# Kernel optimization log

Measured on AMD Instinct MI355X. Metric: run time of the kernel, lower is better.

The kernel has to match this reference:

```python
import jax, jax.numpy as jnp
import numpy as np

B, T, N = 8, 100, 100000
MARGIN = 0.1
THRESHOLD = 0.5
BIG = 1.0e9


def setup_inputs() -> dict:
    key = jax.random.key(0)
    k0, k1, k2, k3, k4 = jax.random.split(key, 5)
    outputs = jax.random.normal(k0, (B, T, 3), dtype=jnp.float32)
    c2ws = jax.random.normal(k1, (B, 4, 4), dtype=jnp.float32)
    scene_scales = jax.random.uniform(k2, (B,), dtype=jnp.float32)
    means = jax.random.normal(k3, (N, 3), dtype=jnp.float32)
    scales = jax.random.uniform(k4, (N, 3), dtype=jnp.float32)
    return {"outputs": outputs, "c2ws": c2ws, "scene_scales": scene_scales,
            "means": means, "scales": scales}


def reference(outputs, c2ws, scene_scales, means, scales):
    # per-splat max radius (precomputed in torch __init__)
    maxsplatrad = jnp.max(scales, axis=1)                      # [N]
    # world transform: aff = R * scene_scale, trans = translation
    aff = c2ws[:, :3, :3] * scene_scales[:, None, None]        # [B,3,3]
    trans = c2ws[:, :3, 3]                                     # [B,3]
    # baddbmm(trans, outputs, aff.mT) == outputs @ aff^T + trans
    retrajs = jnp.einsum('btd,bed->bte', outputs, aff) + trans[:, None, :]  # [B,T,3]
    # axis-aligned bbox of each trajectory, expanded by threshold
    thres = THRESHOLD * scene_scales[0]
    uvals = jnp.max(retrajs, axis=1) + thres                   # [B,3]
    lvals = jnp.min(retrajs, axis=1) - thres                   # [B,3]
    # bbox filter: which splats fall inside each trajectory bbox
    inside = jnp.all((means[None, :, :] >= lvals[:, None, :]) &
                     (means[None, :, :] <= uvals[:, None, :]), axis=2)  # [B,N]
    # pairwise distances via ||a-b||^2 = |a|^2 + |b|^2 - 2 a.b (avoids [B,T,N,3])
    r2 = jnp.sum(retrajs * retrajs, axis=-1)                   # [B,T]
    m2 = jnp.sum(means * means, axis=-1)                       # [N]
    cross = jnp.einsum('btd,nd->btn', retrajs, means)          # [B,T,N]
    d2 = r2[:, :, None] + m2[None, None, :] - 2.0 * cross
    dist = jnp.sqrt(jnp.maximum(d2, 0.0))
    resdists = dist - maxsplatrad[None, None, :] - MARGIN      # [B,T,N]
    # scatter_reduce amin with include_self=False and 1e9 default ==
    # masked min over splats; pairs not inside bbox never scattered -> BIG
    masked = jnp.where(inside[:, None, :], resdists, BIG)
    collosses = jnp.min(masked, axis=2)                        # [B,T]
    return jnp.sum(jax.nn.relu(-collosses)) / (B * T)
```

## Files before the change

kernel.cpp:

```cpp
#include <hip/hip_runtime.h>

constexpr int   B_ = 8;
constexpr int   T_ = 100;
constexpr int   NPAIRS = B_ * T_;
constexpr int   N_ = 100000;
constexpr float MARGIN_ = 0.1f;
constexpr float THRESHOLD_ = 0.5f;
constexpr float BIG_ = 1000000000.0f;

constexpr int PER   = 98;
constexpr int NBLK  = 1024;
constexpr int NSLOT = 1024;
constexpr int KCH   = 16;
constexpr int NRED  = NBLK / KCH;

constexpr size_t RES_OFF  = 0;
constexpr size_t KEYS_OFF = RES_OFF + (size_t)NBLK * NSLOT * 4;
constexpr size_t CNT_OFF  = KEYS_OFF + (size_t)NSLOT * 4;

__device__ __forceinline__ float fsqrt(float x) { return __builtin_amdgcn_sqrtf(x); }

__device__ __forceinline__ unsigned fkey(float f) {
    unsigned u = __float_as_uint(f);
    return (u & 0x80000000u) ? ~u : (u | 0x80000000u);
}

__global__ __launch_bounds__(256) void k_main(const float* __restrict__ outputs,
                                              const float* __restrict__ c2ws,
                                              const float* __restrict__ ss,
                                              const float* __restrict__ means,
                                              const float* __restrict__ scales,
                                              char* __restrict__ ws) {
    __shared__ float  re_s[NPAIRS * 3];
    __shared__ float  bounds_s[48];
    __shared__ float4 rec_s[PER * 3];
    int tid = threadIdx.x;

    if (blockIdx.x == 0) {
        unsigned* keys = (unsigned*)(ws + KEYS_OFF);
        keys[tid]       = fkey(BIG_);
        keys[tid + 256] = fkey(BIG_);
        keys[tid + 512] = fkey(BIG_);
        keys[tid + 768] = fkey(BIG_);
        if (tid == 0) *(unsigned*)(ws + CNT_OFF) = 0;
    }

    for (int p = tid; p < NPAIRS; p += 256) {
        int b = p / T_;
        float s = ss[b];
        const float* o = outputs + p * 3;
        float o0 = o[0], o1 = o[1], o2 = o[2];
        const float* c = c2ws + b * 16;
#pragma unroll
        for (int e = 0; e < 3; e++) {
            re_s[p * 3 + e] =
                (o0 * c[e * 4 + 0] + o1 * c[e * 4 + 1] + o2 * c[e * 4 + 2]) * s + c[e * 4 + 3];
        }
    }
    __syncthreads();

    if (tid < 24) {
        int b = tid / 3, e = tid - b * 3;
        float mx = -3.4e38f, mn = 3.4e38f;
        for (int t = 0; t < T_; t++) {
            float v = re_s[(b * T_ + t) * 3 + e];
            mx = fmaxf(mx, v);
            mn = fminf(mn, v);
        }
        float thres = THRESHOLD_ * ss[0];
        bounds_s[b * 3 + e]      = mn - thres;
        bounds_s[24 + b * 3 + e] = mx + thres;
    }
    __syncthreads();

    float4 q0, q1, q2, q3;
    {
        float4* qs[4] = {&q0, &q1, &q2, &q3};
#pragma unroll
        for (int j = 0; j < 4; j++) {
            int g = tid + j * 256;
            int bb = g >> 7, r = g & 127;
            float4 q = make_float4(0.f, 0.f, 0.f, 0.f);
            if (r < T_) {
                int p = bb * T_ + r;
                q = make_float4(re_s[p * 3 + 0], re_s[p * 3 + 1], re_s[p * 3 + 2], 0.f);
            }
            *qs[j] = q;
        }
    }
    if (tid < PER) {
        int n = blockIdx.x * PER + tid;
        float mx = 0.f, my = 0.f, mz = 0.f;
        float e0, e1, e2, e3, e4, e5, e6, e7;
        if (n < N_) {
            mx = means[(size_t)n * 3 + 0];
            my = means[(size_t)n * 3 + 1];
            mz = means[(size_t)n * 3 + 2];
            float msr = fmaxf(fmaxf(scales[(size_t)n * 3 + 0], scales[(size_t)n * 3 + 1]),
                              scales[(size_t)n * 3 + 2]) + MARGIN_;
            float e[8];
#pragma unroll
            for (int b = 0; b < 8; b++) {
                bool in = (mx >= bounds_s[b * 3 + 0]) & (mx <= bounds_s[24 + b * 3 + 0]) &
                          (my >= bounds_s[b * 3 + 1]) & (my <= bounds_s[24 + b * 3 + 1]) &
                          (mz >= bounds_s[b * 3 + 2]) & (mz <= bounds_s[24 + b * 3 + 2]);
                e[b] = in ? msr : -BIG_;
            }
            e0 = e[0]; e1 = e[1]; e2 = e[2]; e3 = e[3];
            e4 = e[4]; e5 = e[5]; e6 = e[6]; e7 = e[7];
        } else {
            e0 = e1 = e2 = e3 = e4 = e5 = e6 = e7 = -BIG_;
        }
        rec_s[tid * 3 + 0] = make_float4(mx, my, mz, 0.f);
        rec_s[tid * 3 + 1] = make_float4(e0, e2, e4, e6);
        rec_s[tid * 3 + 2] = make_float4(e1, e3, e5, e7);
    }
    __syncthreads();

    int effidx = 1 + ((__builtin_amdgcn_readfirstlane(tid) >> 7) & 1);

    float mn0 = BIG_, mn1 = BIG_, mn2 = BIG_, mn3 = BIG_;
#pragma unroll 2
    for (int i = 0; i < PER; i++) {
        float4 pos = rec_s[i * 3];
        float4 ef  = rec_s[i * 3 + effidx];
        float dx, dy, dz, d2;
        dx = q0.x - pos.x; dy = q0.y - pos.y; dz = q0.z - pos.z;
        d2 = fmaf(dz, dz, fmaf(dy, dy, dx * dx));
        mn0 = fminf(mn0, fsqrt(d2) - ef.x);
        dx = q1.x - pos.x; dy = q1.y - pos.y; dz = q1.z - pos.z;
        d2 = fmaf(dz, dz, fmaf(dy, dy, dx * dx));
        mn1 = fminf(mn1, fsqrt(d2) - ef.y);
        dx = q2.x - pos.x; dy = q2.y - pos.y; dz = q2.z - pos.z;
        d2 = fmaf(dz, dz, fmaf(dy, dy, dx * dx));
        mn2 = fminf(mn2, fsqrt(d2) - ef.z);
        dx = q3.x - pos.x; dy = q3.y - pos.y; dz = q3.z - pos.z;
        d2 = fmaf(dz, dz, fmaf(dy, dy, dx * dx));
        mn3 = fminf(mn3, fsqrt(d2) - ef.w);
    }

    float* res = (float*)(ws + RES_OFF) + (size_t)blockIdx.x * NSLOT;
    res[tid]       = mn0;
    res[tid + 256] = mn1;
    res[tid + 512] = mn2;
    res[tid + 768] = mn3;
}

__global__ __launch_bounds__(256) void k_red(const char* __restrict__ wsc,
                                             char* __restrict__ ws,
                                             float* __restrict__ out) {
    __shared__ int   isLast;
    __shared__ float wsum[4];
    int tid = threadIdx.x;
    const float* res  = (const float*)(wsc + RES_OFF);
    unsigned*    keys = (unsigned*)(ws + KEYS_OFF);
    unsigned*    cnt  = (unsigned*)(ws + CNT_OFF);

    const float* row = res + (size_t)blockIdx.x * KCH * NSLOT;
    float mn0 = BIG_, mn1 = BIG_, mn2 = BIG_, mn3 = BIG_;
#pragma unroll
    for (int i = 0; i < KCH; i++) {
        mn0 = fminf(mn0, row[tid]);
        mn1 = fminf(mn1, row[tid + 256]);
        mn2 = fminf(mn2, row[tid + 512]);
        mn3 = fminf(mn3, row[tid + 768]);
        row += NSLOT;
    }
    atomicMin(&keys[tid],       fkey(mn0));
    atomicMin(&keys[tid + 256], fkey(mn1));
    atomicMin(&keys[tid + 512], fkey(mn2));
    atomicMin(&keys[tid + 768], fkey(mn3));

    __threadfence();
    if (tid == 0) isLast = (atomicAdd(cnt, 1u) == (unsigned)(NRED - 1));
    __syncthreads();
    if (isLast) {
        __threadfence();
        float acc = 0.f;
        for (int s = tid; s < NSLOT; s += 256) {
            if ((s & 127) < T_) {
                unsigned k = __hip_atomic_load(&keys[s], __ATOMIC_RELAXED, __HIP_MEMORY_SCOPE_AGENT);
                unsigned u = (k & 0x80000000u) ? (k ^ 0x80000000u) : ~k;
                acc += fmaxf(0.f, -__uint_as_float(u));
            }
        }
#pragma unroll
        for (int off = 32; off; off >>= 1) acc += __shfl_down(acc, off, 64);
        if ((tid & 63) == 0) wsum[tid >> 6] = acc;
        __syncthreads();
        if (tid == 0)
            out[0] = (wsum[0] + wsum[1] + wsum[2] + wsum[3]) * (1.0f / (float)NPAIRS);
    }
}

extern "C" void kernel_launch(void* const* d_in, const int* in_sizes, int n_in,
                              void* d_out, int out_size, void* d_ws, size_t ws_size,
                              hipStream_t stream) {
    const float* outputs = (const float*)d_in[0];
    const float* c2ws    = (const float*)d_in[1];
    const float* ss      = (const float*)d_in[2];
    const float* means   = (const float*)d_in[3];
    const float* scales  = (const float*)d_in[4];
    float* out = (float*)d_out;
    char*  ws  = (char*)d_ws;

    hipLaunchKernelGGL(k_main, dim3(NBLK), dim3(256), 0, stream,
                       outputs, c2ws, ss, means, scales, ws);
    hipLaunchKernelGGL(k_red, dim3(NRED), dim3(256), 0, stream, (const char*)ws, ws, out);
}
```

Baseline: 96.78 us.

## Skip sqrt via squared-radius test and track clamped max violation

The per-pair minimum becomes a maximum of the clamped collision depth (radius minus distance, floored at zero). This is legal because only relu(-min) is needed in the end. Each candidate splat is first tested by comparing squared distance against squared radius, and the sqrt and max work runs only when some lane in the wavefront has a hit. Since the values are now non-negative, the reduction can use a plain uint atomicMax on the float bits, with no order-preserving key transform. The cost is more shared memory per splat (five float4s instead of three) and a divergent branch on every iteration.

```diff
diff --git a/kernel.cpp b/kernel.cpp
--- a/kernel.cpp
+++ b/kernel.cpp
@@ -19,11 +19,6 @@
 constexpr size_t CNT_OFF  = KEYS_OFF + (size_t)NSLOT * 4;
 
 __device__ __forceinline__ float fsqrt(float x) { return __builtin_amdgcn_sqrtf(x); }
-
-__device__ __forceinline__ unsigned fkey(float f) {
-    unsigned u = __float_as_uint(f);
-    return (u & 0x80000000u) ? ~u : (u | 0x80000000u);
-}
 
 __global__ __launch_bounds__(256) void k_main(const float* __restrict__ outputs,
                                               const float* __restrict__ c2ws,
@@ -33,15 +28,15 @@
                                               char* __restrict__ ws) {
     __shared__ float  re_s[NPAIRS * 3];
     __shared__ float  bounds_s[48];
-    __shared__ float4 rec_s[PER * 3];
+    __shared__ float4 rec_s[PER * 5];
     int tid = threadIdx.x;
 
     if (blockIdx.x == 0) {
         unsigned* keys = (unsigned*)(ws + KEYS_OFF);
-        keys[tid]       = fkey(BIG_);
-        keys[tid + 256] = fkey(BIG_);
-        keys[tid + 512] = fkey(BIG_);
-        keys[tid + 768] = fkey(BIG_);
+        keys[tid]       = 0u;
+        keys[tid + 256] = 0u;
+        keys[tid + 512] = 0u;
+        keys[tid + 768] = 0u;
         if (tid == 0) *(unsigned*)(ws + CNT_OFF) = 0;
     }
 
@@ -91,59 +86,61 @@
     if (tid < PER) {
         int n = blockIdx.x * PER + tid;
         float mx = 0.f, my = 0.f, mz = 0.f;
-        float e0, e1, e2, e3, e4, e5, e6, e7;
+        float e[8], e2[8];
+#pragma unroll
+        for (int b = 0; b < 8; b++) { e[b] = 0.f; e2[b] = -1.f; }
         if (n < N_) {
             mx = means[(size_t)n * 3 + 0];
             my = means[(size_t)n * 3 + 1];
             mz = means[(size_t)n * 3 + 2];
             float msr = fmaxf(fmaxf(scales[(size_t)n * 3 + 0], scales[(size_t)n * 3 + 1]),
                               scales[(size_t)n * 3 + 2]) + MARGIN_;
-            float e[8];
 #pragma unroll
             for (int b = 0; b < 8; b++) {
                 bool in = (mx >= bounds_s[b * 3 + 0]) & (mx <= bounds_s[24 + b * 3 + 0]) &
                           (my >= bounds_s[b * 3 + 1]) & (my <= bounds_s[24 + b * 3 + 1]) &
                           (mz >= bounds_s[b * 3 + 2]) & (mz <= bounds_s[24 + b * 3 + 2]);
-                e[b] = in ? msr : -BIG_;
+                if (in) { e[b] = msr; e2[b] = msr * msr; }
             }
-            e0 = e[0]; e1 = e[1]; e2 = e[2]; e3 = e[3];
-            e4 = e[4]; e5 = e[5]; e6 = e[6]; e7 = e[7];
-        } else {
-            e0 = e1 = e2 = e3 = e4 = e5 = e6 = e7 = -BIG_;
-        }
-        rec_s[tid * 3 + 0] = make_float4(mx, my, mz, 0.f);
-        rec_s[tid * 3 + 1] = make_float4(e0, e2, e4, e6);
-        rec_s[tid * 3 + 2] = make_float4(e1, e3, e5, e7);
-    }
-    __syncthreads();
-
-    int effidx = 1 + ((__builtin_amdgcn_readfirstlane(tid) >> 7) & 1);
-
-    float mn0 = BIG_, mn1 = BIG_, mn2 = BIG_, mn3 = BIG_;
-#pragma unroll 2
+        }
+        rec_s[tid * 5 + 0] = make_float4(mx, my, mz, 0.f);
+        rec_s[tid * 5 + 1] = make_float4(e[0], e[2], e[4], e[6]);
+        rec_s[tid * 5 + 2] = make_float4(e[1], e[3], e[5], e[7]);
+        rec_s[tid * 5 + 3] = make_float4(e2[0], e2[2], e2[4], e2[6]);
+        rec_s[tid * 5 + 4] = make_float4(e2[1], e2[3], e2[5], e2[7]);
+    }
+    __syncthreads();
+
+    int wsel = (__builtin_amdgcn_readfirstlane(tid) >> 7) & 1;
+
+    float mx0 = 0.f, mx1 = 0.f, mx2 = 0.f, mx3 = 0.f;
     for (int i = 0; i < PER; i++) {
-        float4 pos = rec_s[i * 3];
-        float4 ef  = rec_s[i * 3 + effidx];
-        float dx, dy, dz, d2;
+        float4 pos = rec_s[i * 5];
+        float4 s2  = rec_s[i * 5 + 3 + wsel];
+        float dx, dy, dz;
         dx = q0.x - pos.x; dy = q0.y - pos.y; dz = q0.z - pos.z;
-        d2 = fmaf(dz, dz, fmaf(dy, dy, dx * dx));
-        mn0 = fminf(mn0, fsqrt(d2) - ef.x);
+        float d20 = fmaf(dz, dz, fmaf(dy, dy, dx * dx));
         dx = q1.x - pos.x; dy = q1.y - pos.y; dz = q1.z - pos.z;
-        d2 = fmaf(dz, dz, fmaf(dy, dy, dx * dx));
-        mn1 = fminf(mn1, fsqrt(d2) - ef.y);
+        float d21 = fmaf(dz, dz, fmaf(dy, dy, dx * dx));
         dx = q2.x - pos.x; dy = q2.y - pos.y; dz = q2.z - pos.z;
-        d2 = fmaf(dz, dz, fmaf(dy, dy, dx * dx));
-        mn2 = fminf(mn2, fsqrt(d2) - ef.z);
+        float d22 = fmaf(dz, dz, fmaf(dy, dy, dx * dx));
         dx = q3.x - pos.x; dy = q3.y - pos.y; dz = q3.z - pos.z;
-        d2 = fmaf(dz, dz, fmaf(dy, dy, dx * dx));
-        mn3 = fminf(mn3, fsqrt(d2) - ef.w);
+        float d23 = fmaf(dz, dz, fmaf(dy, dy, dx * dx));
+        bool hit = (d20 < s2.x) | (d21 < s2.y) | (d22 < s2.z) | (d23 < s2.w);
+        if (__any(hit)) {
+            float4 ev = rec_s[i * 5 + 1 + wsel];
+            mx0 = fmaxf(mx0, ev.x - fsqrt(d20));
+            mx1 = fmaxf(mx1, ev.y - fsqrt(d21));
+            mx2 = fmaxf(mx2, ev.z - fsqrt(d22));
+            mx3 = fmaxf(mx3, ev.w - fsqrt(d23));
+        }
     }
 
     float* res = (float*)(ws + RES_OFF) + (size_t)blockIdx.x * NSLOT;
-    res[tid]       = mn0;
-    res[tid + 256] = mn1;
-    res[tid + 512] = mn2;
-    res[tid + 768] = mn3;
+    res[tid]       = mx0;
+    res[tid + 256] = mx1;
+    res[tid + 512] = mx2;
+    res[tid + 768] = mx3;
 }
 
 __global__ __launch_bounds__(256) void k_red(const char* __restrict__ wsc,
@@ -157,19 +154,19 @@
     unsigned*    cnt  = (unsigned*)(ws + CNT_OFF);
 
     const float* row = res + (size_t)blockIdx.x * KCH * NSLOT;
-    float mn0 = BIG_, mn1 = BIG_, mn2 = BIG_, mn3 = BIG_;
+    float mx0 = 0.f, mx1 = 0.f, mx2 = 0.f, mx3 = 0.f;
 #pragma unroll
     for (int i = 0; i < KCH; i++) {
-        mn0 = fminf(mn0, row[tid]);
-        mn1 = fminf(mn1, row[tid + 256]);
-        mn2 = fminf(mn2, row[tid + 512]);
-        mn3 = fminf(mn3, row[tid + 768]);
+        mx0 = fmaxf(mx0, row[tid]);
+        mx1 = fmaxf(mx1, row[tid + 256]);
+        mx2 = fmaxf(mx2, row[tid + 512]);
+        mx3 = fmaxf(mx3, row[tid + 768]);
         row += NSLOT;
     }
-    atomicMin(&keys[tid],       fkey(mn0));
-    atomicMin(&keys[tid + 256], fkey(mn1));
-    atomicMin(&keys[tid + 512], fkey(mn2));
-    atomicMin(&keys[tid + 768], fkey(mn3));
+    atomicMax(&keys[tid],       __float_as_uint(mx0));
+    atomicMax(&keys[tid + 256], __float_as_uint(mx1));
+    atomicMax(&keys[tid + 512], __float_as_uint(mx2));
+    atomicMax(&keys[tid + 768], __float_as_uint(mx3));
 
     __threadfence();
     if (tid == 0) isLast = (atomicAdd(cnt, 1u) == (unsigned)(NRED - 1));
@@ -180,8 +177,7 @@
         for (int s = tid; s < NSLOT; s += 256) {
             if ((s & 127) < T_) {
                 unsigned k = __hip_atomic_load(&keys[s], __ATOMIC_RELAXED, __HIP_MEMORY_SCOPE_AGENT);
-                unsigned u = (k & 0x80000000u) ? (k ^ 0x80000000u) : ~k;
-                acc += fmaxf(0.f, -__uint_as_float(u));
+                acc += __uint_as_float(k);
             }
         }
 #pragma unroll
```

After: 108.9 us. 12.5% more time.
